# Performance work log

Hardware: AMD Instinct MI355X
Metric: run time of the kernel (lower is better)

The kernel has to match this reference:

```python
import jax, jax.numpy as jnp
import numpy as np

_EPS = 0.001
_NINF = jnp.finfo(jnp.float32).min

B, LU, LE, D, H, HD = 4, 1024, 1024, 512, 8, 64


def setup_inputs() -> dict:
    ks = jax.random.split(jax.random.key(0), 16)
    w = 1.0 / np.sqrt(D)
    inp = {
        'u_enc': jax.random.normal(ks[0], (B, LU, D), jnp.float32),
        'e_enc': jax.random.normal(ks[1], (B, LE, D), jnp.float32),
        'logit_bpp': jax.random.normal(ks[2], (LU, LE), jnp.float32),
        'ue_mask': jax.random.bernoulli(ks[3], 0.9, (B, 1, LU, LE)),
        'eu_mask': jax.random.bernoulli(ks[4], 0.9, (B, 1, LE, LU)),
        'wq_k': jax.random.normal(ks[5], (D, H, HD), jnp.float32) * w,
        'wq_b': jnp.zeros((H, HD), jnp.float32),
        'wk_k': jax.random.normal(ks[6], (D, H, HD), jnp.float32) * w,
        'wk_b': jnp.zeros((H, HD), jnp.float32),
        'wv_k': jax.random.normal(ks[7], (D, H, HD), jnp.float32) * w,
        'wv_b': jnp.zeros((H, HD), jnp.float32),
        'wo_k': jax.random.normal(ks[8], (H, HD, D), jnp.float32) * (1.0 / np.sqrt(H * HD)),
        'wo_b': jnp.zeros((D,), jnp.float32),
        'bpp_w': jnp.float32(1.0),
        'bpp_b': jnp.float32(0.0),
    }
    return inp


def reference(u_enc, e_enc, logit_bpp, ue_mask, eu_mask,
              wq_k, wq_b, wk_k, wk_b, wv_k, wv_b, wo_k, wo_b,
              bpp_w, bpp_b):
    scale = jnp.reciprocal(jnp.sqrt(jnp.float32(HD)))
    # projections: [B, L, D] @ [D, H, HD] -> [B, L, H, HD]
    q_u = scale * (jnp.einsum('bld,dhk->blhk', u_enc, wq_k) + wq_b)
    q_e = scale * (jnp.einsum('bld,dhk->blhk', e_enc, wq_k) + wq_b)
    k_u = jnp.einsum('bld,dhk->blhk', u_enc, wk_k) + wk_b
    k_e = jnp.einsum('bld,dhk->blhk', e_enc, wk_k) + wk_b

    bpp = bpp_w * logit_bpp + bpp_b                 # [LU, LE]
    bpp_t = bpp.T                                   # [LE, LU]

    # scores: [B, H, Q, K]
    ue_w = jnp.einsum('bqhd,bkhd->bhqk', q_u, k_e) + bpp[None, None]
    eu_w = jnp.einsum('bqhd,bkhd->bhqk', q_e, k_u) + bpp_t[None, None]

    ue_w = jax.nn.softmax(ue_w + (~ue_mask) * _NINF + _EPS, axis=-1)
    eu_w = jax.nn.softmax(eu_w + (~eu_mask) * _NINF + _EPS, axis=-1)

    # deterministic path: no dropout; post-softmax re-mask
    ue_w = ue_mask * ue_w
    eu_w = eu_mask * eu_w

    v_u = jnp.einsum('bld,dhk->blhk', u_enc, wv_k) + wv_b
    v_e = jnp.einsum('bld,dhk->blhk', e_enc, wv_k) + wv_b

    u_ctx = jnp.einsum('bhqk,bkhd->bqhd', ue_w, v_e)
    e_ctx = jnp.einsum('bhqk,bkhd->bqhd', eu_w, v_u)

    u_update = jnp.einsum('bqhd,hde->bqe', u_ctx, wo_k) + wo_b
    e_update = jnp.einsum('bqhd,hde->bqe', e_ctx, wo_k) + wo_b
    return (u_update, e_update)
```

## Files before the change

kernel.cpp:

```cpp
#include <hip/hip_runtime.h>
#include <hip/hip_bf16.h>
#include <cstdint>

typedef unsigned short u16;
typedef __attribute__((ext_vector_type(8))) short short8;
typedef __attribute__((ext_vector_type(4))) float floatx4;

#define MFMA16(a, b, c) __builtin_amdgcn_mfma_f32_16x16x32_bf16(a, b, c, 0, 0, 0)
#define LOG2E 1.4426950408889634f

__device__ __forceinline__ float fast_exp2(float x) {
#if __has_builtin(__builtin_amdgcn_exp2f)
  return __builtin_amdgcn_exp2f(x);
#else
  return exp2f(x);
#endif
}
__device__ __forceinline__ u16 f2bf(float v) {
  union { float f; unsigned u; } x; x.f = v;
  unsigned r = x.u + 0x7FFF + ((x.u >> 16) & 1);
  return (u16)(r >> 16);
}
__device__ __forceinline__ float bf2f(u16 v) {
  union { unsigned u; float f; } x; x.u = ((unsigned)v) << 16; return x.f;
}
__device__ __forceinline__ void gload_lds16(const u16* g, u16* l) {
  __builtin_amdgcn_global_load_lds(
      (const __attribute__((address_space(1))) unsigned int*)(g),
      (__attribute__((address_space(3))) unsigned int*)(l), 16, 0, 0);
}

__global__ __launch_bounds__(256) void prep(
    const float* __restrict__ u, const float* __restrict__ e,
    const float* __restrict__ wq, const float* __restrict__ wk,
    const float* __restrict__ wv, const float* __restrict__ wo,
    const float* __restrict__ bq, const float* __restrict__ bk,
    const float* __restrict__ bv, const float* __restrict__ bo,
    const float* __restrict__ bpp,
    u16* __restrict__ ab, u16* __restrict__ Wt,
    float* __restrict__ bppT, float* __restrict__ bias_all) {
  __shared__ float tl[32][33];
  const int bid = blockIdx.x, t = threadIdx.x;
  if (bid < 4096) {
    int half = bid >> 11;
    int i = ((bid & 2047) * 256 + t) * 4;
    const float* s = half ? e : u;
    float4 v = *(const float4*)(s + i);
    ushort4 o = make_ushort4(f2bf(v.x), f2bf(v.y), f2bf(v.z), f2bf(v.w));
    *(ushort4*)(ab + (size_t)half * 2097152 + i) = o;
  } else if (bid < 5120) {
    int i = bid - 4096;
    int z = i >> 8, rem = i & 255;
    const float* src = z == 0 ? wq : z == 1 ? wk : z == 2 ? wv : wo;
    float scale = z == 0 ? 0.125f * LOG2E : 1.0f;
    u16* dst = Wt + (size_t)z * 262144;
    int k0 = (rem & 15) * 32, n0 = (rem >> 4) * 32;
    int tx = t & 31, ty = t >> 5;
#pragma unroll
    for (int j = 0; j < 32; j += 8) tl[ty + j][tx] = src[(size_t)(k0 + ty + j) * 512 + n0 + tx];
    __syncthreads();
#pragma unroll
    for (int j = 0; j < 32; j += 8)
      dst[(size_t)(n0 + ty + j) * 512 + k0 + tx] = f2bf(scale * tl[tx][ty + j]);
  } else if (bid < 6144) {
    int i = bid - 5120;
    int a0 = (i & 31) * 32, b0 = (i >> 5) * 32;
    int tx = t & 31, ty = t >> 5;
#pragma unroll
    for (int j = 0; j < 32; j += 8) tl[ty + j][tx] = bpp[(size_t)(b0 + ty + j) * 1024 + a0 + tx];
    __syncthreads();
#pragma unroll
    for (int j = 0; j < 32; j += 8) bppT[(size_t)(a0 + ty + j) * 1024 + b0 + tx] = tl[tx][ty + j];
  } else {
    int n = (bid - 6144) * 256 + t;
    float val = n < 512 ? 0.125f * LOG2E * bq[n]
              : n < 1024 ? bk[n - 512]
              : n < 1536 ? bv[n - 1024] : bo[n - 1536];
    bias_all[n] = val;
  }
}

__global__ __launch_bounds__(256) void build_bm(
    const int* __restrict__ mu, const int* __restrict__ me,
    const float* __restrict__ bpp, const float* __restrict__ bppT,
    const float* __restrict__ bw_p, const float* __restrict__ bb_p,
    u16* __restrict__ bm) {
  __shared__ u16 lds[2048];
  const int kcpair = blockIdx.x, q16 = blockIdx.y;
  const int side = blockIdx.z >> 2, b = blockIdx.z & 3;
  const int* mask = side ? me : mu;
  const float* bp = side ? bppT : bpp;
  const float sw = (*bw_p) * LOG2E, sb = (*bb_p) * LOG2E;
  const int t = threadIdx.x;
#pragma unroll
  for (int ii = 0; ii < 2; ++ii) {
    int s = t + ii * 256;
    int q = s >> 5;
    int kq = (s & 31) * 4;
    int qg = q16 * 16 + q, kg = kcpair * 128 + kq;
    int4 mv = *(const int4*)(mask + ((size_t)b * 1024 + qg) * 1024 + kg);
    float4 bv = *(const float4*)(bp + (size_t)qg * 1024 + kg);
    int kb = (kq >> 4) & 3, kc_loc = kq >> 6;
    int quad = q >> 2, r = q & 3;
    u16 o[4];
    o[0] = f2bf(mv.x ? sw * bv.x + sb : -1e30f);
    o[1] = f2bf(mv.y ? sw * bv.y + sb : -1e30f);
    o[2] = f2bf(mv.z ? sw * bv.z + sb : -1e30f);
    o[3] = f2bf(mv.w ? sw * bv.w + sb : -1e30f);
#pragma unroll
    for (int j = 0; j < 4; ++j) {
      int l15 = (kq & 15) + j;
      lds[kc_loc * 1024 + (quad * 16 + l15) * 16 + kb * 4 + r] = o[j];
    }
  }
  __syncthreads();
  u16* dst = bm + ((((size_t)side * 4 + b) * 64 + q16) * 16 + kcpair * 2) * 1024;
  *(short8*)(dst + t * 8) = *(const short8*)&lds[t * 8];
}

template <int MODE>
__global__ __launch_bounds__(256) void gemm_mfma(
    const u16* __restrict__ A, const u16* __restrict__ Bt,
    const float* __restrict__ bias, float* __restrict__ outf,
    u16* __restrict__ q_o, u16* __restrict__ k_o, u16* __restrict__ v_o) {
  __shared__ u16 As[128 * 32];
  __shared__ u16 Bs[128 * 32];
  const int t = threadIdx.x, lane = t & 63, wave = t >> 6;
  const int l15 = lane & 15, quad = lane >> 4;
  const int wy = wave >> 1, wx = wave & 1;
  const int m0 = blockIdx.x * 128, n0 = blockIdx.y * 128;
  const int K = 512;

  floatx4 zero4 = {0.f, 0.f, 0.f, 0.f};
  floatx4 acc[4][4];
#pragma unroll
  for (int mi = 0; mi < 4; ++mi)
#pragma unroll
    for (int ni = 0; ni < 4; ++ni) acc[mi][ni] = zero4;

  for (int k0 = 0; k0 < K; k0 += 32) {
    __syncthreads();
    {
      int s = t;
#pragma unroll
      for (int i = 0; i < 2; ++i, s += 256) {
        int row = s >> 2, seg = s & 3;
        gload_lds16(A + (size_t)(m0 + row) * K + k0 + seg * 8, &As[s * 8]);
      }
      s = t;
#pragma unroll
      for (int i = 0; i < 2; ++i, s += 256) {
        int row = s >> 2, seg = s & 3;
        gload_lds16(Bt + (size_t)(n0 + row) * K + k0 + seg * 8, &Bs[s * 8]);
      }
    }
    __syncthreads();
    short8 af[4], bf[4];
#pragma unroll
    for (int mi = 0; mi < 4; ++mi)
      af[mi] = *(const short8*)&As[(wy * 64 + mi * 16 + l15) * 32 + quad * 8];
#pragma unroll
    for (int ni = 0; ni < 4; ++ni)
      bf[ni] = *(const short8*)&Bs[(wx * 64 + ni * 16 + l15) * 32 + quad * 8];
#pragma unroll
    for (int mi = 0; mi < 4; ++mi)
#pragma unroll
      for (int ni = 0; ni < 4; ++ni) acc[mi][ni] = MFMA16(af[mi], bf[ni], acc[mi][ni]);
  }

#pragma unroll
  for (int mi = 0; mi < 4; ++mi)
#pragma unroll
    for (int ni = 0; ni < 4; ++ni) {
      int n = n0 + wx * 64 + ni * 16 + l15;
      float bv = bias[n];
#pragma unroll
      for (int r = 0; r < 4; ++r) {
        int m = m0 + wy * 64 + mi * 16 + quad * 4 + r;
        float v = acc[mi][ni][r] + bv;
        if (MODE == 1) {
          outf[(size_t)m * 512 + n] = v;
        } else {
          int sel = n >> 9, c = n & 511;
          u16 hv = f2bf(v);
          if (sel == 0) q_o[(size_t)m * 512 + c] = hv;
          else if (sel == 1) k_o[(size_t)m * 512 + c] = hv;
          else v_o[(size_t)m * 512 + c] = hv;
        }
      }
    }
}

__global__ __launch_bounds__(256) void vt_trans(const u16* __restrict__ v_all,
                                                u16* __restrict__ vt_all) {
  __shared__ u16 tl[64][72];
  int z = blockIdx.z, half = z >> 2, b = z & 3, h = blockIdx.y, l0 = blockIdx.x * 64;
  const u16* src = v_all + (size_t)half * 2097152;
  u16* dst = vt_all + (size_t)half * 2097152;
  int t = threadIdx.x;
#pragma unroll
  for (int i = 0; i < 2; ++i) {
    int s = t + i * 256, row = s >> 3, seg = s & 7;
    *(short8*)&tl[row][seg * 8] =
        *(const short8*)(src + (size_t)(b * 1024 + l0 + row) * 512 + h * 64 + seg * 8);
  }
  __syncthreads();
#pragma unroll
  for (int i = 0; i < 2; ++i) {
    int s = t + i * 256, hd = s >> 3, seg = s & 7;
    u16 tmp[8];
#pragma unroll
    for (int j = 0; j < 8; ++j) tmp[j] = tl[seg * 8 + j][hd];
    *(short8*)(dst + ((size_t)(b * 8 + h) * 64 + hd) * 1024 + l0 + seg * 8) =
        *(const short8*)tmp;
  }
}

__global__ __launch_bounds__(256, 4) void attn_mfma(
    const u16* __restrict__ q_all, const u16* __restrict__ k_all,
    const u16* __restrict__ vt_all, const u16* __restrict__ bm_all,
    u16* __restrict__ ctx_all) {
  __shared__ u16 Ks[2][64 * 64];
  __shared__ u16 Vs[2][64 * 64];
  __shared__ u16 Ps[4][16 * 64];
  const int t = threadIdx.x, lane = t & 63, wave = t >> 6;
  const int l15 = lane & 15, quad = lane >> 4;

  const int f = blockIdx.x;
  const int g = f & 7, r0 = f >> 3;
  const int combo = g * 8 + (r0 >> 4);
  const int x = r0 & 15;
  const int side = combo >> 5, b = (combo >> 3) & 3, h = combo & 7;

  const size_t HALF = 2097152;
  const u16* Q = q_all + side * HALF;
  const u16* K = k_all + (1 - side) * HALF;
  const u16* Vt = vt_all + (1 - side) * HALF;
  const u16* bm = bm_all + side * (size_t)4194304;
  u16* ctx = ctx_all + side * HALF;
  const int qbase = x * 64 + wave * 16;
  const int q16g = qbase >> 4;

  short8 qa0, qa1;
  {
    const u16* qp = Q + (size_t)(b * 1024 + qbase + l15) * 512 + h * 64 + quad * 8;
    qa0 = *(const short8*)qp;
    qa1 = *(const short8*)(qp + 32);
  }

  short8 bones;
#pragma unroll
  for (int j = 0; j < 8; ++j) bones[j] = (short)0x3F80;

  floatx4 O[4], O5;
  O5 = (floatx4){0.f, 0.f, 0.f, 0.f};
#pragma unroll
  for (int nb = 0; nb < 4; ++nb) O[nb] = (floatx4){0.f, 0.f, 0.f, 0.f};

#define STAGE(buf, k0)                                                             \
  {                                                                                \
    _Pragma("unroll") for (int i = 0; i < 2; ++i) {                                \
      int s = t + i * 256, row = s >> 3, pseg = s & 7, lseg = pseg ^ (row & 7);    \
      gload_lds16(K + (size_t)(b * 1024 + (k0) + row) * 512 + h * 64 + lseg * 8,   \
                  &Ks[buf][s * 8]);                                                \
      gload_lds16(Vt + ((size_t)(b * 8 + h) * 64 + row) * 1024 + (k0) + lseg * 8,  \
                  &Vs[buf][s * 8]);                                                \
    }                                                                              \
  }

  STAGE(0, 0)

  for (int it = 0; it < 16; ++it) {
    const int cur = it & 1;
    __syncthreads();
    if (it < 15) STAGE(cur ^ 1, it * 64 + 64)

    short8 bmv0, bmv1;
    {
      const u16* bp = bm + ((((size_t)b * 64 + q16g) * 16 + it) * 64 + lane) * 16;
      bmv0 = *(const short8*)bp;
      bmv1 = *(const short8*)(bp + 8);
    }

    floatx4 S[4];
#pragma unroll
    for (int kb = 0; kb < 4; ++kb) S[kb] = (floatx4){-64.f, -64.f, -64.f, -64.f};
#pragma unroll
    for (int kb = 0; kb < 4; ++kb) {
      int krow = kb * 16 + l15;
      short8 b0 = *(const short8*)&Ks[cur][krow * 64 + ((quad ^ (krow & 7)) * 8)];
      short8 b1 = *(const short8*)&Ks[cur][krow * 64 + (((4 + quad) ^ (krow & 7)) * 8)];
      S[kb] = MFMA16(qa0, b0, S[kb]);
      S[kb] = MFMA16(qa1, b1, S[kb]);
    }

    u16* ps = &Ps[wave][0];
#pragma unroll
    for (int kb = 0; kb < 4; ++kb) {
      float pv[4];
#pragma unroll
      for (int r = 0; r < 4; ++r) {
        int i = kb * 4 + r;
        float bmf = bf2f((u16)((i < 8) ? bmv0[i] : bmv1[i - 8]));
        pv[r] = fast_exp2(S[kb][r] + bmf);
      }
      int seg = kb * 2 + (l15 >> 3);
#pragma unroll
      for (int r = 0; r < 4; r += 2) {
        union { __hip_bfloat162 hh; u16 u[2]; } cv;
        cv.hh = __float22bfloat162_rn(make_float2(pv[r], pv[r + 1]));
        int row0 = quad * 4 + r, row1 = row0 + 1;
        ps[row0 * 64 + ((seg ^ (row0 & 7)) * 8) + (l15 & 7)] = cv.u[0];
        ps[row1 * 64 + ((seg ^ (row1 & 7)) * 8) + (l15 & 7)] = cv.u[1];
      }
    }
    short8 pa0 = *(const short8*)&ps[l15 * 64 + ((quad ^ (l15 & 7)) * 8)];
    short8 pa1 = *(const short8*)&ps[l15 * 64 + (((4 + quad) ^ (l15 & 7)) * 8)];

#pragma unroll
    for (int nb = 0; nb < 4; ++nb) {
      int vrow = nb * 16 + l15;
      short8 v0 = *(const short8*)&Vs[cur][vrow * 64 + ((quad ^ (vrow & 7)) * 8)];
      short8 v1 = *(const short8*)&Vs[cur][vrow * 64 + (((4 + quad) ^ (vrow & 7)) * 8)];
      O[nb] = MFMA16(pa0, v0, O[nb]);
      O[nb] = MFMA16(pa1, v1, O[nb]);
    }
    O5 = MFMA16(pa0, bones, O5);
    O5 = MFMA16(pa1, bones, O5);
  }

#pragma unroll
  for (int r = 0; r < 4; ++r) {
    float l = O5[r];
    float inv = l > 0.f ? 1.f / l : 0.f;
    int qd = qbase + quad * 4 + r;
    u16* cp = ctx + (size_t)(b * 1024 + qd) * 512 + h * 64;
#pragma unroll
    for (int nb = 0; nb < 4; ++nb) cp[nb * 16 + l15] = f2bf(O[nb][r] * inv);
  }
}

extern "C" void kernel_launch(void* const* d_in, const int* in_sizes, int n_in,
                              void* d_out, int out_size, void* d_ws, size_t ws_size,
                              hipStream_t stream) {
  const float* u_enc = (const float*)d_in[0];
  const float* e_enc = (const float*)d_in[1];
  const float* logit_bpp = (const float*)d_in[2];
  const int* ue_mask = (const int*)d_in[3];
  const int* eu_mask = (const int*)d_in[4];
  const float* wq_k = (const float*)d_in[5];
  const float* wq_b = (const float*)d_in[6];
  const float* wk_k = (const float*)d_in[7];
  const float* wk_b = (const float*)d_in[8];
  const float* wv_k = (const float*)d_in[9];
  const float* wv_b = (const float*)d_in[10];
  const float* wo_k = (const float*)d_in[11];
  const float* wo_b = (const float*)d_in[12];
  const float* bpp_w = (const float*)d_in[13];
  const float* bpp_b = (const float*)d_in[14];

  float* out = (float*)d_out;

  u16* ws16 = (u16*)d_ws;
  u16* ab    = ws16;
  u16* Wt    = ab + 4194304;
  u16* q_all = Wt + 1048576;
  u16* k_all = q_all + 4194304;
  u16* v_all = k_all + 4194304;
  u16* ctx   = v_all + 4194304;
  u16* bm    = ctx + 4194304;
  float* bppT = (float*)(bm + 8388608);
  float* bias_all = bppT + 1048576;
  u16* vt = ab;

  prep<<<6152, 256, 0, stream>>>(u_enc, e_enc, wq_k, wk_k, wv_k, wo_k,
                                 wq_b, wk_b, wv_b, wo_b, logit_bpp,
                                 ab, Wt, bppT, bias_all);
  build_bm<<<dim3(8, 64, 8), 256, 0, stream>>>(ue_mask, eu_mask, logit_bpp, bppT,
                                               bpp_w, bpp_b, bm);
  gemm_mfma<0><<<dim3(64, 12), 256, 0, stream>>>(ab, Wt, bias_all, nullptr,
                                                 q_all, k_all, v_all);
  vt_trans<<<dim3(16, 8, 8), 256, 0, stream>>>(v_all, vt);
  attn_mfma<<<1024, 256, 0, stream>>>(q_all, k_all, vt, bm, ctx);
  gemm_mfma<1><<<dim3(64, 4), 256, 0, stream>>>(ctx, Wt + 786432, bias_all + 1536,
                                                out, nullptr, nullptr, nullptr);
}
```

Baseline: 203.4 us.

## Double query rows per wave, transpose P in registers, fuse mask build into prep

The attention kernel now has each wave handle 32 query rows (two 16-row slices), so every K and V fragment read from LDS feeds twice as many MFMAs. It also computes transposed scores so that P can be rearranged in registers with permlane swaps rather than bounced through LDS. The output epilogue is staged through LDS to allow vectorized 16-byte stores. Separately, the bias/mask build is merged into the prep kernel and transposes bpp on the fly, which removes the bppT buffer and one launch. The trade-offs are higher register pressure (the occupancy hint was dropped) and half as many blocks in the attention grid.

New measurement: 197.3 us. 1.03x faster.

```diff
diff --git a/kernel.cpp b/kernel.cpp
--- a/kernel.cpp
+++ b/kernel.cpp
@@ -28,6 +28,36 @@
   __builtin_amdgcn_global_load_lds(
       (const __attribute__((address_space(1))) unsigned int*)(g),
       (__attribute__((address_space(3))) unsigned int*)(l), 16, 0, 0);
+}
+
+#if __has_builtin(__builtin_amdgcn_permlane32_swap) && __has_builtin(__builtin_amdgcn_permlane16_swap)
+#define HAVE_PL 1
+#endif
+__device__ __forceinline__ void plswap32(unsigned& x, unsigned& y) {
+#ifdef HAVE_PL
+  auto r = __builtin_amdgcn_permlane32_swap(x, y, false, false);
+  x = r[0]; y = r[1];
+#else
+  unsigned sx = (unsigned)__shfl_xor((int)x, 32, 64);
+  unsigned sy = (unsigned)__shfl_xor((int)y, 32, 64);
+  bool hi = (threadIdx.x & 32) != 0;
+  unsigned nx = hi ? sy : x;
+  unsigned ny = hi ? y : sx;
+  x = nx; y = ny;
+#endif
+}
+__device__ __forceinline__ void plswap16(unsigned& x, unsigned& y) {
+#ifdef HAVE_PL
+  auto r = __builtin_amdgcn_permlane16_swap(x, y, false, false);
+  x = r[0]; y = r[1];
+#else
+  unsigned sx = (unsigned)__shfl_xor((int)x, 16, 64);
+  unsigned sy = (unsigned)__shfl_xor((int)y, 16, 64);
+  bool odd = (threadIdx.x & 16) != 0;
+  unsigned nx = odd ? sy : x;
+  unsigned ny = odd ? y : sx;
+  x = nx; y = ny;
+#endif
 }
 
 __global__ __launch_bounds__(256) void prep(
@@ -37,9 +67,12 @@
     const float* __restrict__ bq, const float* __restrict__ bk,
     const float* __restrict__ bv, const float* __restrict__ bo,
     const float* __restrict__ bpp,
+    const int* __restrict__ mu, const int* __restrict__ me,
+    const float* __restrict__ bw_p, const float* __restrict__ bb_p,
     u16* __restrict__ ab, u16* __restrict__ Wt,
-    float* __restrict__ bppT, float* __restrict__ bias_all) {
-  __shared__ float tl[32][33];
+    float* __restrict__ bias_all, u16* __restrict__ bm) {
+  __shared__ float smemf[2176];
+  __shared__ u16 smemo[2048];
   const int bid = blockIdx.x, t = threadIdx.x;
   if (bid < 4096) {
     int half = bid >> 11;
@@ -56,66 +89,67 @@
     u16* dst = Wt + (size_t)z * 262144;
     int k0 = (rem & 15) * 32, n0 = (rem >> 4) * 32;
     int tx = t & 31, ty = t >> 5;
+    float (*tl)[33] = (float(*)[33])smemf;
 #pragma unroll
     for (int j = 0; j < 32; j += 8) tl[ty + j][tx] = src[(size_t)(k0 + ty + j) * 512 + n0 + tx];
     __syncthreads();
 #pragma unroll
     for (int j = 0; j < 32; j += 8)
       dst[(size_t)(n0 + ty + j) * 512 + k0 + tx] = f2bf(scale * tl[tx][ty + j]);
-  } else if (bid < 6144) {
-    int i = bid - 5120;
-    int a0 = (i & 31) * 32, b0 = (i >> 5) * 32;
-    int tx = t & 31, ty = t >> 5;
-#pragma unroll
-    for (int j = 0; j < 32; j += 8) tl[ty + j][tx] = bpp[(size_t)(b0 + ty + j) * 1024 + a0 + tx];
-    __syncthreads();
-#pragma unroll
-    for (int j = 0; j < 32; j += 8) bppT[(size_t)(a0 + ty + j) * 1024 + b0 + tx] = tl[tx][ty + j];
-  } else {
-    int n = (bid - 6144) * 256 + t;
+  } else if (bid < 5128) {
+    int n = (bid - 5120) * 256 + t;
     float val = n < 512 ? 0.125f * LOG2E * bq[n]
               : n < 1024 ? bk[n - 512]
               : n < 1536 ? bv[n - 1024] : bo[n - 1536];
     bias_all[n] = val;
-  }
-}
-
-__global__ __launch_bounds__(256) void build_bm(
-    const int* __restrict__ mu, const int* __restrict__ me,
-    const float* __restrict__ bpp, const float* __restrict__ bppT,
-    const float* __restrict__ bw_p, const float* __restrict__ bb_p,
-    u16* __restrict__ bm) {
-  __shared__ u16 lds[2048];
-  const int kcpair = blockIdx.x, q16 = blockIdx.y;
-  const int side = blockIdx.z >> 2, b = blockIdx.z & 3;
-  const int* mask = side ? me : mu;
-  const float* bp = side ? bppT : bpp;
-  const float sw = (*bw_p) * LOG2E, sb = (*bb_p) * LOG2E;
-  const int t = threadIdx.x;
-#pragma unroll
-  for (int ii = 0; ii < 2; ++ii) {
-    int s = t + ii * 256;
-    int q = s >> 5;
-    int kq = (s & 31) * 4;
-    int qg = q16 * 16 + q, kg = kcpair * 128 + kq;
-    int4 mv = *(const int4*)(mask + ((size_t)b * 1024 + qg) * 1024 + kg);
-    float4 bv = *(const float4*)(bp + (size_t)qg * 1024 + kg);
-    int kb = (kq >> 4) & 3, kc_loc = kq >> 6;
-    int quad = q >> 2, r = q & 3;
-    u16 o[4];
-    o[0] = f2bf(mv.x ? sw * bv.x + sb : -1e30f);
-    o[1] = f2bf(mv.y ? sw * bv.y + sb : -1e30f);
-    o[2] = f2bf(mv.z ? sw * bv.z + sb : -1e30f);
-    o[3] = f2bf(mv.w ? sw * bv.w + sb : -1e30f);
-#pragma unroll
-    for (int j = 0; j < 4; ++j) {
-      int l15 = (kq & 15) + j;
-      lds[kc_loc * 1024 + (quad * 16 + l15) * 16 + kb * 4 + r] = o[j];
-    }
-  }
-  __syncthreads();
-  u16* dst = bm + ((((size_t)side * 4 + b) * 64 + q16) * 16 + kcpair * 2) * 1024;
-  *(short8*)(dst + t * 8) = *(const short8*)&lds[t * 8];
+  } else {
+    int i = bid - 5128;
+    int kcpair = i & 7, q16 = (i >> 3) & 63, sb = i >> 9;
+    int side = sb >> 2, b = sb & 3;
+    const int* mask = side ? me : mu;
+    const float sw = (*bw_p) * LOG2E, sb2 = (*bb_p) * LOG2E;
+    if (side) {
+#pragma unroll
+      for (int ii = 0; ii < 2; ++ii) {
+        int s = t + ii * 256;
+        int rowk = s >> 2, c4 = (s & 3) * 4;
+        float4 v = *(const float4*)(bpp + (size_t)(kcpair * 128 + rowk) * 1024 + q16 * 16 + c4);
+        smemf[rowk * 17 + c4 + 0] = v.x;
+        smemf[rowk * 17 + c4 + 1] = v.y;
+        smemf[rowk * 17 + c4 + 2] = v.z;
+        smemf[rowk * 17 + c4 + 3] = v.w;
+      }
+    }
+    __syncthreads();
+#pragma unroll
+    for (int ii = 0; ii < 2; ++ii) {
+      int s = t + ii * 256;
+      int q_loc = s >> 5;
+      int kq = (s & 31) * 4;
+      int qg = q16 * 16 + q_loc;
+      int4 mv = *(const int4*)(mask + ((size_t)b * 1024 + qg) * 1024 + kcpair * 128 + kq);
+      float bvv[4];
+      if (side) {
+#pragma unroll
+        for (int j = 0; j < 4; ++j) bvv[j] = smemf[(kq + j) * 17 + q_loc];
+      } else {
+        float4 v = *(const float4*)(bpp + (size_t)qg * 1024 + kcpair * 128 + kq);
+        bvv[0] = v.x; bvv[1] = v.y; bvv[2] = v.z; bvv[3] = v.w;
+      }
+      int mm[4] = {mv.x, mv.y, mv.z, mv.w};
+      int kc_loc = kq >> 6, k_loc = kq & 63;
+      int kb = k_loc >> 4, within = k_loc & 15;
+      int quad = within >> 2;
+      int lane = q_loc + 16 * quad;
+      u16 o[4];
+#pragma unroll
+      for (int j = 0; j < 4; ++j) o[j] = f2bf(mm[j] ? sw * bvv[j] + sb2 : -1e30f);
+      *(ushort4*)&smemo[kc_loc * 1024 + lane * 16 + kb * 4] = *(const ushort4*)o;
+    }
+    __syncthreads();
+    u16* dst = bm + (((size_t)sb * 64 + q16) * 16 + kcpair * 2) * 1024;
+    *(short8*)(dst + t * 8) = *(const short8*)&smemo[t * 8];
+  }
 }
 
 template <int MODE>
@@ -216,20 +250,20 @@
   }
 }
 
-__global__ __launch_bounds__(256, 4) void attn_mfma(
+__global__ __launch_bounds__(256) void attn_mfma(
     const u16* __restrict__ q_all, const u16* __restrict__ k_all,
     const u16* __restrict__ vt_all, const u16* __restrict__ bm_all,
     u16* __restrict__ ctx_all) {
   __shared__ u16 Ks[2][64 * 64];
   __shared__ u16 Vs[2][64 * 64];
-  __shared__ u16 Ps[4][16 * 64];
+  __shared__ u16 epi[4][32 * 72];
   const int t = threadIdx.x, lane = t & 63, wave = t >> 6;
   const int l15 = lane & 15, quad = lane >> 4;
 
   const int f = blockIdx.x;
   const int g = f & 7, r0 = f >> 3;
-  const int combo = g * 8 + (r0 >> 4);
-  const int x = r0 & 15;
+  const int combo = g * 8 + (r0 >> 3);
+  const int x = r0 & 7;
   const int side = combo >> 5, b = (combo >> 3) & 3, h = combo & 7;
 
   const size_t HALF = 2097152;
@@ -238,24 +272,29 @@
   const u16* Vt = vt_all + (1 - side) * HALF;
   const u16* bm = bm_all + side * (size_t)4194304;
   u16* ctx = ctx_all + side * HALF;
-  const int qbase = x * 64 + wave * 16;
+  const int qbase = x * 128 + wave * 32;
   const int q16g = qbase >> 4;
 
-  short8 qa0, qa1;
-  {
-    const u16* qp = Q + (size_t)(b * 1024 + qbase + l15) * 512 + h * 64 + quad * 8;
-    qa0 = *(const short8*)qp;
-    qa1 = *(const short8*)(qp + 32);
-  }
-
-  short8 bones;
-#pragma unroll
-  for (int j = 0; j < 8; ++j) bones[j] = (short)0x3F80;
-
-  floatx4 O[4], O5;
-  O5 = (floatx4){0.f, 0.f, 0.f, 0.f};
-#pragma unroll
-  for (int nb = 0; nb < 4; ++nb) O[nb] = (floatx4){0.f, 0.f, 0.f, 0.f};
+  short8 qb[2][2];
+#pragma unroll
+  for (int s = 0; s < 2; ++s) {
+    const u16* qp = Q + (size_t)(b * 1024 + qbase + s * 16 + l15) * 512 + h * 64 + quad * 8;
+    qb[s][0] = *(const short8*)qp;
+    qb[s][1] = *(const short8*)(qp + 32);
+  }
+
+  short8 onesA;
+#pragma unroll
+  for (int j = 0; j < 8; ++j) onesA[j] = (short)0x3F80;
+
+  floatx4 Oc[4][2];
+  floatx4 Dacc[2];
+#pragma unroll
+  for (int s = 0; s < 2; ++s) {
+    Dacc[s] = (floatx4){0.f, 0.f, 0.f, 0.f};
+#pragma unroll
+    for (int nb = 0; nb < 4; ++nb) Oc[nb][s] = (floatx4){0.f, 0.f, 0.f, 0.f};
+  }
 
 #define STAGE(buf, k0)                                                             \
   {                                                                                \
@@ -275,68 +314,98 @@
     __syncthreads();
     if (it < 15) STAGE(cur ^ 1, it * 64 + 64)
 
-    short8 bmv0, bmv1;
-    {
-      const u16* bp = bm + ((((size_t)b * 64 + q16g) * 16 + it) * 64 + lane) * 16;
-      bmv0 = *(const short8*)bp;
-      bmv1 = *(const short8*)(bp + 8);
-    }
-
-    floatx4 S[4];
-#pragma unroll
-    for (int kb = 0; kb < 4; ++kb) S[kb] = (floatx4){-64.f, -64.f, -64.f, -64.f};
+    short8 bmv[2][2];
+#pragma unroll
+    for (int s = 0; s < 2; ++s) {
+      const u16* bp = bm + ((((size_t)b * 64 + q16g + s) * 16 + it) * 64 + lane) * 16;
+      bmv[s][0] = *(const short8*)bp;
+      bmv[s][1] = *(const short8*)(bp + 8);
+    }
+
+    floatx4 St[2][4];
+#pragma unroll
+    for (int s = 0; s < 2; ++s)
+#pragma unroll
+      for (int kb = 0; kb < 4; ++kb) St[s][kb] = (floatx4){-64.f, -64.f, -64.f, -64.f};
 #pragma unroll
     for (int kb = 0; kb < 4; ++kb) {
       int krow = kb * 16 + l15;
-      short8 b0 = *(const short8*)&Ks[cur][krow * 64 + ((quad ^ (krow & 7)) * 8)];
-      short8 b1 = *(const short8*)&Ks[cur][krow * 64 + (((4 + quad) ^ (krow & 7)) * 8)];
-      S[kb] = MFMA16(qa0, b0, S[kb]);
-      S[kb] = MFMA16(qa1, b1, S[kb]);
-    }
-
-    u16* ps = &Ps[wave][0];
-#pragma unroll
-    for (int kb = 0; kb < 4; ++kb) {
-      float pv[4];
-#pragma unroll
-      for (int r = 0; r < 4; ++r) {
-        int i = kb * 4 + r;
-        float bmf = bf2f((u16)((i < 8) ? bmv0[i] : bmv1[i - 8]));
-        pv[r] = fast_exp2(S[kb][r] + bmf);
-      }
-      int seg = kb * 2 + (l15 >> 3);
-#pragma unroll
-      for (int r = 0; r < 4; r += 2) {
-        union { __hip_bfloat162 hh; u16 u[2]; } cv;
-        cv.hh = __float22bfloat162_rn(make_float2(pv[r], pv[r + 1]));
-        int row0 = quad * 4 + r, row1 = row0 + 1;
-        ps[row0 * 64 + ((seg ^ (row0 & 7)) * 8) + (l15 & 7)] = cv.u[0];
-        ps[row1 * 64 + ((seg ^ (row1 & 7)) * 8) + (l15 & 7)] = cv.u[1];
-      }
-    }
-    short8 pa0 = *(const short8*)&ps[l15 * 64 + ((quad ^ (l15 & 7)) * 8)];
-    short8 pa1 = *(const short8*)&ps[l15 * 64 + (((4 + quad) ^ (l15 & 7)) * 8)];
+      short8 kf0 = *(const short8*)&Ks[cur][krow * 64 + ((quad ^ (krow & 7)) * 8)];
+      short8 kf1 = *(const short8*)&Ks[cur][krow * 64 + (((4 + quad) ^ (krow & 7)) * 8)];
+#pragma unroll
+      for (int s = 0; s < 2; ++s) {
+        St[s][kb] = MFMA16(kf0, qb[s][0], St[s][kb]);
+        St[s][kb] = MFMA16(kf1, qb[s][1], St[s][kb]);
+      }
+    }
+
+    unsigned pka[2][4], pkb[2][4];
+#pragma unroll
+    for (int s = 0; s < 2; ++s)
+#pragma unroll
+      for (int kb = 0; kb < 4; ++kb) {
+        float pv[4];
+#pragma unroll
+        for (int r = 0; r < 4; ++r) {
+          int i = kb * 4 + r;
+          float bmf = bf2f((u16)((i < 8) ? bmv[s][0][i] : bmv[s][1][i - 8]));
+          pv[r] = fast_exp2(St[s][kb][r] + bmf);
+        }
+        union { __hip_bfloat162 h; unsigned u; } c0, c1;
+        c0.h = __float22bfloat162_rn(make_float2(pv[0], pv[1]));
+        c1.h = __float22bfloat162_rn(make_float2(pv[2], pv[3]));
+        pka[s][kb] = c0.u;
+        pkb[s][kb] = c1.u;
+      }
+
+    short8 Pb[2][2];
+#pragma unroll
+    for (int s = 0; s < 2; ++s)
+#pragma unroll
+      for (int ks = 0; ks < 2; ++ks) {
+        unsigned a0 = pka[s][2 * ks], a1 = pka[s][2 * ks + 1];
+        unsigned b0 = pkb[s][2 * ks], b1 = pkb[s][2 * ks + 1];
+        plswap32(a0, a1); plswap16(a0, a1);
+        plswap32(b0, b1); plswap16(b0, b1);
+        union { short8 s8; unsigned u[4]; } fb;
+        fb.u[0] = a0; fb.u[1] = b0; fb.u[2] = a1; fb.u[3] = b1;
+        Pb[s][ks] = fb.s8;
+        Dacc[s] = MFMA16(onesA, fb.s8, Dacc[s]);
+      }
 
 #pragma unroll
     for (int nb = 0; nb < 4; ++nb) {
       int vrow = nb * 16 + l15;
-      short8 v0 = *(const short8*)&Vs[cur][vrow * 64 + ((quad ^ (vrow & 7)) * 8)];
-      short8 v1 = *(const short8*)&Vs[cur][vrow * 64 + (((4 + quad) ^ (vrow & 7)) * 8)];
-      O[nb] = MFMA16(pa0, v0, O[nb]);
-      O[nb] = MFMA16(pa1, v1, O[nb]);
-    }
-    O5 = MFMA16(pa0, bones, O5);
-    O5 = MFMA16(pa1, bones, O5);
-  }
-
-#pragma unroll
-  for (int r = 0; r < 4; ++r) {
-    float l = O5[r];
-    float inv = l > 0.f ? 1.f / l : 0.f;
-    int qd = qbase + quad * 4 + r;
-    u16* cp = ctx + (size_t)(b * 1024 + qd) * 512 + h * 64;
-#pragma unroll
-    for (int nb = 0; nb < 4; ++nb) cp[nb * 16 + l15] = f2bf(O[nb][r] * inv);
+#pragma unroll
+      for (int ks = 0; ks < 2; ++ks) {
+        short8 vf = *(const short8*)&Vs[cur][vrow * 64 + ((((ks * 4 + quad)) ^ (vrow & 7)) * 8)];
+        Oc[nb][0] = MFMA16(vf, Pb[0][ks], Oc[nb][0]);
+        Oc[nb][1] = MFMA16(vf, Pb[1][ks], Oc[nb][1]);
+      }
+    }
+  }
+
+  u16* eb = &epi[wave][0];
+#pragma unroll
+  for (int s = 0; s < 2; ++s) {
+    float dv = Dacc[s][0];
+    float inv = dv > 0.f ? 1.f / dv : 0.f;
+#pragma unroll
+    for (int nb = 0; nb < 4; ++nb) {
+      union { __hip_bfloat162 h; unsigned u; } w0, w1;
+      w0.h = __float22bfloat162_rn(make_float2(Oc[nb][s][0] * inv, Oc[nb][s][1] * inv));
+      w1.h = __float22bfloat162_rn(make_float2(Oc[nb][s][2] * inv, Oc[nb][s][3] * inv));
+      union { unsigned u[2]; unsigned long long ull; } pk;
+      pk.u[0] = w0.u; pk.u[1] = w1.u;
+      *(unsigned long long*)&eb[(s * 16 + l15) * 72 + nb * 16 + quad * 4] = pk.ull;
+    }
+  }
+#pragma unroll
+  for (int p = 0; p < 4; ++p) {
+    int row = p * 8 + (lane >> 3);
+    int cs = (lane & 7) * 8;
+    short8 v = *(const short8*)&eb[row * 72 + cs];
+    *(short8*)(ctx + (size_t)(b * 1024 + qbase + row) * 512 + h * 64 + cs) = v;
   }
 }
 
@@ -369,19 +438,17 @@
   u16* v_all = k_all + 4194304;
   u16* ctx   = v_all + 4194304;
   u16* bm    = ctx + 4194304;
-  float* bppT = (float*)(bm + 8388608);
-  float* bias_all = bppT + 1048576;
+  float* bias_all = (float*)(bm + 8388608);
   u16* vt = ab;
 
-  prep<<<6152, 256, 0, stream>>>(u_enc, e_enc, wq_k, wk_k, wv_k, wo_k,
+  prep<<<9224, 256, 0, stream>>>(u_enc, e_enc, wq_k, wk_k, wv_k, wo_k,
                                  wq_b, wk_b, wv_b, wo_b, logit_bpp,
-                                 ab, Wt, bppT, bias_all);
-  build_bm<<<dim3(8, 64, 8), 256, 0, stream>>>(ue_mask, eu_mask, logit_bpp, bppT,
-                                               bpp_w, bpp_b, bm);
+                                 ue_mask, eu_mask, bpp_w, bpp_b,
+                                 ab, Wt, bias_all, bm);
   gemm_mfma<0><<<dim3(64, 12), 256, 0, stream>>>(ab, Wt, bias_all, nullptr,
                                                  q_all, k_all, v_all);
   vt_trans<<<dim3(16, 8, 8), 256, 0, stream>>>(v_all, vt);
-  attn_mfma<<<1024, 256, 0, stream>>>(q_all, k_all, vt, bm, ctx);
+  attn_mfma<<<512, 256, 0, stream>>>(q_all, k_all, vt, bm, ctx);
   gemm_mfma<1><<<dim3(64, 4), 256, 0, stream>>>(ctx, Wt + 786432, bias_all + 1536,
                                                 out, nullptr, nullptr, nullptr);
 }
```
